# Performance work log

Hardware: AMD Instinct MI355X
Metric: run time of the kernel (lower is better)

## Reference

```python
import jax, jax.numpy as jnp
import numpy as np

NUM_NODES = 10000
NUM_EDGES = 640000
IN_CH = 128
HID = 128
OUT_CH = 1


def setup_inputs() -> dict:
    key = jax.random.key(0)
    ks = jax.random.split(key, 12)
    x = jax.random.normal(ks[0], (NUM_NODES, IN_CH), dtype=jnp.float32)
    edge_index = jax.random.randint(ks[1], (2, NUM_EDGES), 0, NUM_NODES, dtype=jnp.int64)
    edge_weight = jax.random.uniform(ks[2], (NUM_EDGES,), dtype=jnp.float32)
    s1 = 1.0 / np.sqrt(IN_CH)
    s2 = 1.0 / np.sqrt(HID)
    W1 = jax.random.uniform(ks[3], (HID, IN_CH), minval=-s1, maxval=s1, dtype=jnp.float32)
    b1 = jnp.zeros((HID,), dtype=jnp.float32)
    W2 = jax.random.uniform(ks[4], (HID, HID), minval=-s2, maxval=s2, dtype=jnp.float32)
    b2 = jnp.zeros((HID,), dtype=jnp.float32)
    sc = 1.0 / np.sqrt(HID * 3)
    conv_w = jax.random.uniform(ks[5], (HID, HID, 3), minval=-sc, maxval=sc, dtype=jnp.float32)
    conv_b = jax.random.uniform(ks[6], (HID,), minval=-sc, maxval=sc, dtype=jnp.float32)
    fc_w = jax.random.uniform(ks[7], (OUT_CH, HID), minval=-s2, maxval=s2, dtype=jnp.float32)
    fc_b = jax.random.uniform(ks[8], (OUT_CH,), minval=-s2, maxval=s2, dtype=jnp.float32)
    return {"x": x, "edge_index": edge_index, "edge_weight": edge_weight,
            "W1": W1, "b1": b1, "W2": W2, "b2": b2,
            "conv_w": conv_w, "conv_b": conv_b, "fc_w": fc_w, "fc_b": fc_b}


def _gcn_conv(x, row, col, norm, W, b):
    # PyG GCNConv: linear (no bias in lin), normalized scatter-add, then bias
    xw = x @ W.T                                   # [N, out]
    msg = xw[row] * norm[:, None]                  # gather + edge scale [E, out]
    out = jax.ops.segment_sum(msg, col, num_segments=NUM_NODES)
    return out + b


def reference(x, edge_index, edge_weight, W1, b1, W2, b2, conv_w, conv_b, fc_w, fc_b):
    # gcn_norm with self-loops (fill_value=1.0)
    loop = jnp.arange(NUM_NODES, dtype=edge_index.dtype)
    row = jnp.concatenate([edge_index[0], loop])
    col = jnp.concatenate([edge_index[1], loop])
    w = jnp.concatenate([edge_weight, jnp.ones((NUM_NODES,), dtype=edge_weight.dtype)])
    deg = jax.ops.segment_sum(w, col, num_segments=NUM_NODES)
    dinv = jnp.where(deg > 0, jax.lax.rsqrt(deg), 0.0)
    norm = dinv[row] * w * dinv[col]

    h = jax.nn.relu(_gcn_conv(x, row, col, norm, W1, b1))
    # dropout is identity in eval mode
    h = jax.nn.relu(_gcn_conv(h, row, col, norm, W2, b2))

    # temporal conv1d over node axis: [N,H] -> [1,H,N]
    hc = h.T[None, :, :]
    hc = jax.lax.conv_general_dilated(hc, conv_w, window_strides=(1,),
                                      padding='SAME',
                                      dimension_numbers=('NCH', 'OIH', 'NCH'))
    hc = hc + conv_b[None, :, None]
    h = hc[0].T                                    # [N, H]

    return (h @ fc_w.T + fc_b).squeeze()           # [N]
```

## Files before the change

kernel.cpp:

```cpp
#include <hip/hip_runtime.h>
#include <hip/hip_bf16.h>

#define N_NODES 10000
#define N_EDGES 640000
#define CH 128
#define NB 128
#define EPB (N_EDGES / NB)
#define NCHUNK 40

__global__ __launch_bounds__(256) void hist_kernel(const int* __restrict__ ei,
                                                   const float* __restrict__ ew,
                                                   int* __restrict__ hist,
                                                   float* __restrict__ dhist) {
    __shared__ int h[N_NODES];
    __shared__ float hf[N_NODES];
    int b = blockIdx.x, t = threadIdx.x;
    for (int i = t; i < N_NODES; i += 256) { h[i] = 0; hf[i] = 0.0f; }
    __syncthreads();
    int e0 = b * EPB;
    for (int i = t; i < EPB; i += 256) {
        int c = ei[N_EDGES + e0 + i];
        float w = ew[e0 + i];
        atomicAdd(&h[c], 1);
        atomicAdd(&hf[c], w);
    }
    __syncthreads();
    for (int i = t; i < N_NODES; i += 256) {
        hist[b * N_NODES + i] = h[i];
        dhist[b * N_NODES + i] = hf[i];
    }
}

__global__ __launch_bounds__(256) void reduce_kernel(const int* __restrict__ hist,
        const float* __restrict__ dhist, int* __restrict__ tot,
        float* __restrict__ dinv, int* __restrict__ csum,
        const float* __restrict__ conv_w, const float* __restrict__ conv_b,
        const float* __restrict__ fc_w, const float* __restrict__ fc_b,
        float* __restrict__ vbuf, float* __restrict__ c0) {
    int blk = blockIdx.x, t = threadIdx.x;
    if (blk == NCHUNK) {
        for (int i = t; i <= 384; i += 256) {
            if (i < 384) {
                float s = 0.0f;
                for (int o = 0; o < CH; ++o) s += fc_w[o] * conv_w[o * 384 + i];
                vbuf[i] = s;
            } else {
                float s = fc_b[0];
                for (int o = 0; o < CH; ++o) s += fc_w[o] * conv_b[o];
                *c0 = s;
            }
        }
        return;
    }
    int n = blk * 256 + t;
    int c = 0;
    if (n < N_NODES) {
        float d = 0.0f;
        #pragma unroll 4
        for (int b = 0; b < NB; ++b) {
            c += hist[b * N_NODES + n];
            d += dhist[b * N_NODES + n];
        }
        tot[n] = c;
        dinv[n] = rsqrtf(d + 1.0f);
    }
    __shared__ int wred[4];
    int lane = t & 63, wave = t >> 6;
    int s = c;
    #pragma unroll
    for (int off = 32; off > 0; off >>= 1) s += __shfl_down(s, off, 64);
    if (lane == 0) wred[wave] = s;
    __syncthreads();
    if (t == 0) csum[blk] = wred[0] + wred[1] + wred[2] + wred[3];
}

__global__ __launch_bounds__(256) void bofs_kernel(int* __restrict__ hist,
        const int* __restrict__ tot, const int* __restrict__ csum,
        int* __restrict__ offs) {
    __shared__ int lds_csum[NCHUNK];
    __shared__ int wsum[4];
    int blk = blockIdx.x, t = threadIdx.x;
    if (t < NCHUNK) lds_csum[t] = csum[t];
    __syncthreads();
    int base = 0;
    for (int i = 0; i < blk; ++i) base += lds_csum[i];
    int n = blk * 256 + t;
    int v = (n < N_NODES) ? tot[n] : 0;
    int lane = t & 63, wave = t >> 6;
    int s = v;
    #pragma unroll
    for (int off = 1; off < 64; off <<= 1) {
        int u = __shfl_up(s, off, 64);
        if (lane >= off) s += u;
    }
    if (lane == 63) wsum[wave] = s;
    __syncthreads();
    int wbase = 0;
    for (int i = 0; i < wave; ++i) wbase += wsum[i];
    if (n < N_NODES) {
        int run = base + wbase + s - v;
        offs[n] = run;
        for (int b = 0; b < NB; ++b) {
            int h = hist[b * N_NODES + n];
            hist[b * N_NODES + n] = run;
            run += h;
        }
    }
}

__global__ __launch_bounds__(256) void scatter_kernel(const int* __restrict__ ei,
        const float* __restrict__ ew, const float* __restrict__ dinv,
        const int* __restrict__ bofs, int2* __restrict__ erec) {
    __shared__ int cur[N_NODES];
    __shared__ float di[N_NODES];
    int b = blockIdx.x, t = threadIdx.x;
    for (int i = t; i < N_NODES; i += 256) {
        cur[i] = bofs[b * N_NODES + i];
        di[i] = dinv[i];
    }
    __syncthreads();
    int e0 = b * EPB;
    for (int i = t; i < EPB; i += 256) {
        int e = e0 + i;
        int r = ei[e];
        int c = ei[N_EDGES + e];
        int p = atomicAdd(&cur[c], 1);
        float v = di[r] * ew[e] * di[c];
        erec[p] = make_int2(r, __float_as_int(v));
    }
}

__global__ __launch_bounds__(256) void gemm128_kernel(const float* __restrict__ A,
                                                      const float* __restrict__ W,
                                                      float* __restrict__ out, int M) {
    __shared__ float As[32][68];
    __shared__ float Ws[32][132];
    int tid = threadIdx.x;
    int tx = tid & 31;
    int ty = tid >> 5;
    int row0 = blockIdx.x * 64;
    float acc[8][4] = {};
    for (int k0 = 0; k0 < 128; k0 += 32) {
        #pragma unroll
        for (int i = 0; i < 8; ++i) {
            int idx = tid + i * 256;
            int r = idx >> 5, k = idx & 31;
            int gr = row0 + r;
            As[k][r] = (gr < M) ? A[gr * CH + k0 + k] : 0.0f;
        }
        #pragma unroll
        for (int i = 0; i < 16; ++i) {
            int idx = tid + i * 256;
            int o = idx >> 5, k = idx & 31;
            Ws[k][o] = W[o * CH + k0 + k];
        }
        __syncthreads();
        #pragma unroll
        for (int kk = 0; kk < 32; ++kk) {
            float a[8], w[4];
            #pragma unroll
            for (int j = 0; j < 8; ++j) a[j] = As[kk][ty * 8 + j];
            #pragma unroll
            for (int c = 0; c < 4; ++c) w[c] = Ws[kk][tx * 4 + c];
            #pragma unroll
            for (int j = 0; j < 8; ++j)
                #pragma unroll
                for (int c = 0; c < 4; ++c)
                    acc[j][c] += a[j] * w[c];
        }
        __syncthreads();
    }
    #pragma unroll
    for (int j = 0; j < 8; ++j) {
        int gr = row0 + ty * 8 + j;
        if (gr < M) {
            float4 v = make_float4(acc[j][0], acc[j][1], acc[j][2], acc[j][3]);
            *reinterpret_cast<float4*>(&out[gr * CH + tx * 4]) = v;
        }
    }
}

__global__ __launch_bounds__(256) void agg_kernel(const float4* __restrict__ xw4,
        const int2* __restrict__ erec, const int* __restrict__ offs,
        const int* __restrict__ cnt, const float* __restrict__ dinv,
        const float4* __restrict__ bias4, float4* __restrict__ out4) {
    int l = threadIdx.x & 31;
    int g = threadIdx.x >> 5;
    int n = blockIdx.x * 8 + g;
    float d = dinv[n];
    float dd = d * d;
    float4 self = xw4[n * 32 + l];
    float4 acc = make_float4(dd * self.x, dd * self.y, dd * self.z, dd * self.w);
    int start = offs[n];
    int num = cnt[n];
    int i = 0;
    for (; i + 8 <= num; i += 8) {
        int2 r[8];
        #pragma unroll
        for (int j = 0; j < 8; ++j) r[j] = erec[start + i + j];
        float4 f[8];
        #pragma unroll
        for (int j = 0; j < 8; ++j) f[j] = xw4[r[j].x * 32 + l];
        #pragma unroll
        for (int j = 0; j < 8; ++j) {
            float v = __int_as_float(r[j].y);
            acc.x += v * f[j].x; acc.y += v * f[j].y;
            acc.z += v * f[j].z; acc.w += v * f[j].w;
        }
    }
    for (; i < num; ++i) {
        int2 r = erec[start + i];
        float4 f = xw4[r.x * 32 + l];
        float v = __int_as_float(r.y);
        acc.x += v * f.x; acc.y += v * f.y; acc.z += v * f.z; acc.w += v * f.w;
    }
    float4 bb = bias4[l];
    acc.x = fmaxf(acc.x + bb.x, 0.0f);
    acc.y = fmaxf(acc.y + bb.y, 0.0f);
    acc.z = fmaxf(acc.z + bb.z, 0.0f);
    acc.w = fmaxf(acc.w + bb.w, 0.0f);
    out4[n * 32 + l] = acc;
}

__global__ __launch_bounds__(128) void convfc_kernel(const float* __restrict__ h,
        const float* __restrict__ v, const float* __restrict__ c0,
        float* __restrict__ out, int N) {
    int n = blockIdx.x;
    int t = threadIdx.x;
    float p = 0.0f;
    if (n > 0)     p += h[(n - 1) * CH + t] * v[t * 3 + 0];
    p += h[n * CH + t] * v[t * 3 + 1];
    if (n < N - 1) p += h[(n + 1) * CH + t] * v[t * 3 + 2];
    #pragma unroll
    for (int off = 32; off > 0; off >>= 1) p += __shfl_down(p, off, 64);
    __shared__ float red[2];
    if ((t & 63) == 0) red[t >> 6] = p;
    __syncthreads();
    if (t == 0) out[n] = red[0] + red[1] + *c0;
}

extern "C" void kernel_launch(void* const* d_in, const int* in_sizes, int n_in,
                              void* d_out, int out_size, void* d_ws, size_t ws_size,
                              hipStream_t stream) {
    const float* x       = (const float*)d_in[0];
    const int*   ei      = (const int*)d_in[1];
    const float* ew      = (const float*)d_in[2];
    const float* W1      = (const float*)d_in[3];
    const float* b1      = (const float*)d_in[4];
    const float* W2      = (const float*)d_in[5];
    const float* b2      = (const float*)d_in[6];
    const float* conv_w  = (const float*)d_in[7];
    const float* conv_b  = (const float*)d_in[8];
    const float* fc_w    = (const float*)d_in[9];
    const float* fc_b    = (const float*)d_in[10];
    float* out = (float*)d_out;

    float* bufA   = (float*)d_ws;
    float* bufB   = bufA + N_NODES * CH;
    int2*  erec   = (int2*)(bufB + N_NODES * CH);
    int*   hist   = (int*)bufA;
    float* dhist  = (float*)erec;
    int*   tot    = (int*)(erec + N_EDGES);
    int*   offs   = tot + N_NODES;
    float* dinv   = (float*)(offs + N_NODES);
    float* vbuf   = dinv + N_NODES;
    float* c0     = vbuf + 384;
    int*   csum   = (int*)(c0 + 1);

    hist_kernel<<<NB, 256, 0, stream>>>(ei, ew, hist, dhist);
    reduce_kernel<<<NCHUNK + 1, 256, 0, stream>>>(hist, dhist, tot, dinv, csum,
                                                  conv_w, conv_b, fc_w, fc_b, vbuf, c0);
    bofs_kernel<<<NCHUNK, 256, 0, stream>>>(hist, tot, csum, offs);
    scatter_kernel<<<NB, 256, 0, stream>>>(ei, ew, dinv, hist, erec);

    const int gemm_grid = (N_NODES + 63) / 64;
    gemm128_kernel<<<gemm_grid, 256, 0, stream>>>(x, W1, bufA, N_NODES);
    agg_kernel<<<N_NODES / 8, 256, 0, stream>>>((const float4*)bufA, erec, offs, tot,
                                                dinv, (const float4*)b1, (float4*)bufB);
    gemm128_kernel<<<gemm_grid, 256, 0, stream>>>(bufB, W2, bufA, N_NODES);
    agg_kernel<<<N_NODES / 8, 256, 0, stream>>>((const float4*)bufA, erec, offs, tot,
                                                dinv, (const float4*)b2, (float4*)bufB);
    convfc_kernel<<<N_NODES, 128, 0, stream>>>(bufB, vbuf, c0, out, N_NODES);
}
```

Before: 227.4 us.

## Fuse all GCN stages into one persistent kernel with grid barriers

Replaces the nine separate kernel launches with a single persistent 256-block kernel that moves between phases using atomic-counter grid barriers. The first GEMM now runs alongside the degree histogram on the blocks that are otherwise idle, and the conv+fc tail is vectorised with float4 loads and 32-lane reductions. The aim is to remove launch gaps and idle tails between the small stages. In exchange, work per phase is limited to 256 blocks, seven spin barriers are added, and correctness depends on all 256 blocks being co-resident.

New measurement: 608.7 us. 2.68x slower.

```diff
diff --git a/kernel.cpp b/kernel.cpp
--- a/kernel.cpp
+++ b/kernel.cpp
@@ -1,144 +1,41 @@
 #include <hip/hip_runtime.h>
-#include <hip/hip_bf16.h>
 
 #define N_NODES 10000
 #define N_EDGES 640000
 #define CH 128
-#define NB 128
-#define EPB (N_EDGES / NB)
+#define NBLK 256
+#define NTHR 256
+#define NHB 128
+#define EPB (N_EDGES / NHB)
 #define NCHUNK 40
-
-__global__ __launch_bounds__(256) void hist_kernel(const int* __restrict__ ei,
-                                                   const float* __restrict__ ew,
-                                                   int* __restrict__ hist,
-                                                   float* __restrict__ dhist) {
-    __shared__ int h[N_NODES];
-    __shared__ float hf[N_NODES];
-    int b = blockIdx.x, t = threadIdx.x;
-    for (int i = t; i < N_NODES; i += 256) { h[i] = 0; hf[i] = 0.0f; }
+#define GTILES 157
+
+union SMem {
+    struct { int h[N_NODES]; float hf[N_NODES]; } hist;
+    struct { int cur[N_NODES]; float di[N_NODES]; } scat;
+    struct { float As[32][68]; float Ws[32][132]; } gemm;
+    struct { int csum[NCHUNK]; int wsum[4]; } scan;
+    int red[4];
+};
+
+__device__ __forceinline__ void gridbar(int* ctr, int target) {
+    __threadfence();
     __syncthreads();
-    int e0 = b * EPB;
-    for (int i = t; i < EPB; i += 256) {
-        int c = ei[N_EDGES + e0 + i];
-        float w = ew[e0 + i];
-        atomicAdd(&h[c], 1);
-        atomicAdd(&hf[c], w);
+    if (threadIdx.x == 0) {
+        atomicAdd(ctr, 1);
+        while (__hip_atomic_load(ctr, __ATOMIC_RELAXED, __HIP_MEMORY_SCOPE_AGENT) < target)
+            __builtin_amdgcn_s_sleep(2);
     }
     __syncthreads();
-    for (int i = t; i < N_NODES; i += 256) {
-        hist[b * N_NODES + i] = h[i];
-        dhist[b * N_NODES + i] = hf[i];
-    }
-}
-
-__global__ __launch_bounds__(256) void reduce_kernel(const int* __restrict__ hist,
-        const float* __restrict__ dhist, int* __restrict__ tot,
-        float* __restrict__ dinv, int* __restrict__ csum,
-        const float* __restrict__ conv_w, const float* __restrict__ conv_b,
-        const float* __restrict__ fc_w, const float* __restrict__ fc_b,
-        float* __restrict__ vbuf, float* __restrict__ c0) {
-    int blk = blockIdx.x, t = threadIdx.x;
-    if (blk == NCHUNK) {
-        for (int i = t; i <= 384; i += 256) {
-            if (i < 384) {
-                float s = 0.0f;
-                for (int o = 0; o < CH; ++o) s += fc_w[o] * conv_w[o * 384 + i];
-                vbuf[i] = s;
-            } else {
-                float s = fc_b[0];
-                for (int o = 0; o < CH; ++o) s += fc_w[o] * conv_b[o];
-                *c0 = s;
-            }
-        }
-        return;
-    }
-    int n = blk * 256 + t;
-    int c = 0;
-    if (n < N_NODES) {
-        float d = 0.0f;
-        #pragma unroll 4
-        for (int b = 0; b < NB; ++b) {
-            c += hist[b * N_NODES + n];
-            d += dhist[b * N_NODES + n];
-        }
-        tot[n] = c;
-        dinv[n] = rsqrtf(d + 1.0f);
-    }
-    __shared__ int wred[4];
-    int lane = t & 63, wave = t >> 6;
-    int s = c;
-    #pragma unroll
-    for (int off = 32; off > 0; off >>= 1) s += __shfl_down(s, off, 64);
-    if (lane == 0) wred[wave] = s;
-    __syncthreads();
-    if (t == 0) csum[blk] = wred[0] + wred[1] + wred[2] + wred[3];
-}
-
-__global__ __launch_bounds__(256) void bofs_kernel(int* __restrict__ hist,
-        const int* __restrict__ tot, const int* __restrict__ csum,
-        int* __restrict__ offs) {
-    __shared__ int lds_csum[NCHUNK];
-    __shared__ int wsum[4];
-    int blk = blockIdx.x, t = threadIdx.x;
-    if (t < NCHUNK) lds_csum[t] = csum[t];
-    __syncthreads();
-    int base = 0;
-    for (int i = 0; i < blk; ++i) base += lds_csum[i];
-    int n = blk * 256 + t;
-    int v = (n < N_NODES) ? tot[n] : 0;
-    int lane = t & 63, wave = t >> 6;
-    int s = v;
-    #pragma unroll
-    for (int off = 1; off < 64; off <<= 1) {
-        int u = __shfl_up(s, off, 64);
-        if (lane >= off) s += u;
-    }
-    if (lane == 63) wsum[wave] = s;
-    __syncthreads();
-    int wbase = 0;
-    for (int i = 0; i < wave; ++i) wbase += wsum[i];
-    if (n < N_NODES) {
-        int run = base + wbase + s - v;
-        offs[n] = run;
-        for (int b = 0; b < NB; ++b) {
-            int h = hist[b * N_NODES + n];
-            hist[b * N_NODES + n] = run;
-            run += h;
-        }
-    }
-}
-
-__global__ __launch_bounds__(256) void scatter_kernel(const int* __restrict__ ei,
-        const float* __restrict__ ew, const float* __restrict__ dinv,
-        const int* __restrict__ bofs, int2* __restrict__ erec) {
-    __shared__ int cur[N_NODES];
-    __shared__ float di[N_NODES];
-    int b = blockIdx.x, t = threadIdx.x;
-    for (int i = t; i < N_NODES; i += 256) {
-        cur[i] = bofs[b * N_NODES + i];
-        di[i] = dinv[i];
-    }
-    __syncthreads();
-    int e0 = b * EPB;
-    for (int i = t; i < EPB; i += 256) {
-        int e = e0 + i;
-        int r = ei[e];
-        int c = ei[N_EDGES + e];
-        int p = atomicAdd(&cur[c], 1);
-        float v = di[r] * ew[e] * di[c];
-        erec[p] = make_int2(r, __float_as_int(v));
-    }
-}
-
-__global__ __launch_bounds__(256) void gemm128_kernel(const float* __restrict__ A,
-                                                      const float* __restrict__ W,
-                                                      float* __restrict__ out, int M) {
-    __shared__ float As[32][68];
-    __shared__ float Ws[32][132];
+    __threadfence();
+}
+
+__device__ __forceinline__ void gemm_tile(const float* __restrict__ A,
+        const float* __restrict__ W, float* __restrict__ out, int tile, SMem& sm) {
     int tid = threadIdx.x;
     int tx = tid & 31;
     int ty = tid >> 5;
-    int row0 = blockIdx.x * 64;
+    int row0 = tile * 64;
     float acc[8][4] = {};
     for (int k0 = 0; k0 < 128; k0 += 32) {
         #pragma unroll
@@ -146,22 +43,22 @@
             int idx = tid + i * 256;
             int r = idx >> 5, k = idx & 31;
             int gr = row0 + r;
-            As[k][r] = (gr < M) ? A[gr * CH + k0 + k] : 0.0f;
+            sm.gemm.As[k][r] = (gr < N_NODES) ? A[gr * CH + k0 + k] : 0.0f;
         }
         #pragma unroll
         for (int i = 0; i < 16; ++i) {
             int idx = tid + i * 256;
             int o = idx >> 5, k = idx & 31;
-            Ws[k][o] = W[o * CH + k0 + k];
+            sm.gemm.Ws[k][o] = W[o * CH + k0 + k];
         }
         __syncthreads();
         #pragma unroll
         for (int kk = 0; kk < 32; ++kk) {
             float a[8], w[4];
             #pragma unroll
-            for (int j = 0; j < 8; ++j) a[j] = As[kk][ty * 8 + j];
-            #pragma unroll
-            for (int c = 0; c < 4; ++c) w[c] = Ws[kk][tx * 4 + c];
+            for (int j = 0; j < 8; ++j) a[j] = sm.gemm.As[kk][ty * 8 + j];
+            #pragma unroll
+            for (int c = 0; c < 4; ++c) w[c] = sm.gemm.Ws[kk][tx * 4 + c];
             #pragma unroll
             for (int j = 0; j < 8; ++j)
                 #pragma unroll
@@ -173,70 +70,215 @@
     #pragma unroll
     for (int j = 0; j < 8; ++j) {
         int gr = row0 + ty * 8 + j;
-        if (gr < M) {
+        if (gr < N_NODES) {
             float4 v = make_float4(acc[j][0], acc[j][1], acc[j][2], acc[j][3]);
             *reinterpret_cast<float4*>(&out[gr * CH + tx * 4]) = v;
         }
     }
 }
 
-__global__ __launch_bounds__(256) void agg_kernel(const float4* __restrict__ xw4,
+__device__ __forceinline__ void agg_phase(const float4* __restrict__ xw4,
         const int2* __restrict__ erec, const int* __restrict__ offs,
         const int* __restrict__ cnt, const float* __restrict__ dinv,
         const float4* __restrict__ bias4, float4* __restrict__ out4) {
     int l = threadIdx.x & 31;
     int g = threadIdx.x >> 5;
-    int n = blockIdx.x * 8 + g;
-    float d = dinv[n];
-    float dd = d * d;
-    float4 self = xw4[n * 32 + l];
-    float4 acc = make_float4(dd * self.x, dd * self.y, dd * self.z, dd * self.w);
-    int start = offs[n];
-    int num = cnt[n];
-    int i = 0;
-    for (; i + 8 <= num; i += 8) {
-        int2 r[8];
-        #pragma unroll
-        for (int j = 0; j < 8; ++j) r[j] = erec[start + i + j];
-        float4 f[8];
-        #pragma unroll
-        for (int j = 0; j < 8; ++j) f[j] = xw4[r[j].x * 32 + l];
-        #pragma unroll
-        for (int j = 0; j < 8; ++j) {
-            float v = __int_as_float(r[j].y);
-            acc.x += v * f[j].x; acc.y += v * f[j].y;
-            acc.z += v * f[j].z; acc.w += v * f[j].w;
-        }
-    }
-    for (; i < num; ++i) {
-        int2 r = erec[start + i];
-        float4 f = xw4[r.x * 32 + l];
-        float v = __int_as_float(r.y);
-        acc.x += v * f.x; acc.y += v * f.y; acc.z += v * f.z; acc.w += v * f.w;
-    }
-    float4 bb = bias4[l];
-    acc.x = fmaxf(acc.x + bb.x, 0.0f);
-    acc.y = fmaxf(acc.y + bb.y, 0.0f);
-    acc.z = fmaxf(acc.z + bb.z, 0.0f);
-    acc.w = fmaxf(acc.w + bb.w, 0.0f);
-    out4[n * 32 + l] = acc;
-}
-
-__global__ __launch_bounds__(128) void convfc_kernel(const float* __restrict__ h,
-        const float* __restrict__ v, const float* __restrict__ c0,
-        float* __restrict__ out, int N) {
-    int n = blockIdx.x;
-    int t = threadIdx.x;
-    float p = 0.0f;
-    if (n > 0)     p += h[(n - 1) * CH + t] * v[t * 3 + 0];
-    p += h[n * CH + t] * v[t * 3 + 1];
-    if (n < N - 1) p += h[(n + 1) * CH + t] * v[t * 3 + 2];
-    #pragma unroll
-    for (int off = 32; off > 0; off >>= 1) p += __shfl_down(p, off, 64);
-    __shared__ float red[2];
-    if ((t & 63) == 0) red[t >> 6] = p;
-    __syncthreads();
-    if (t == 0) out[n] = red[0] + red[1] + *c0;
+    for (int n = blockIdx.x * 8 + g; n < N_NODES; n += NBLK * 8) {
+        float d = dinv[n];
+        float dd = d * d;
+        float4 self = xw4[n * 32 + l];
+        float4 acc = make_float4(dd * self.x, dd * self.y, dd * self.z, dd * self.w);
+        int start = offs[n];
+        int num = cnt[n];
+        int i = 0;
+        for (; i + 8 <= num; i += 8) {
+            int2 r[8];
+            #pragma unroll
+            for (int j = 0; j < 8; ++j) r[j] = erec[start + i + j];
+            float4 f[8];
+            #pragma unroll
+            for (int j = 0; j < 8; ++j) f[j] = xw4[r[j].x * 32 + l];
+            #pragma unroll
+            for (int j = 0; j < 8; ++j) {
+                float v = __int_as_float(r[j].y);
+                acc.x += v * f[j].x; acc.y += v * f[j].y;
+                acc.z += v * f[j].z; acc.w += v * f[j].w;
+            }
+        }
+        for (; i < num; ++i) {
+            int2 r = erec[start + i];
+            float4 f = xw4[r.x * 32 + l];
+            float v = __int_as_float(r.y);
+            acc.x += v * f.x; acc.y += v * f.y; acc.z += v * f.z; acc.w += v * f.w;
+        }
+        float4 bb = bias4[l];
+        acc.x = fmaxf(acc.x + bb.x, 0.0f);
+        acc.y = fmaxf(acc.y + bb.y, 0.0f);
+        acc.z = fmaxf(acc.z + bb.z, 0.0f);
+        acc.w = fmaxf(acc.w + bb.w, 0.0f);
+        out4[n * 32 + l] = acc;
+    }
+}
+
+__global__ void init_ctr_kernel(int* ctr) { if (threadIdx.x == 0) *ctr = 0; }
+
+__global__ __launch_bounds__(NTHR) void mega_kernel(
+        const float* __restrict__ x, const int* __restrict__ ei,
+        const float* __restrict__ ew,
+        const float* __restrict__ W1, const float* __restrict__ b1,
+        const float* __restrict__ W2, const float* __restrict__ b2,
+        const float* __restrict__ conv_w, const float* __restrict__ conv_b,
+        const float* __restrict__ fc_w, const float* __restrict__ fc_b,
+        float* __restrict__ out,
+        float* __restrict__ xw1, float* __restrict__ h1,
+        float* __restrict__ xw2, float* __restrict__ h2,
+        int2* __restrict__ erec, int* __restrict__ hist, float* __restrict__ dhist,
+        int* __restrict__ tot, int* __restrict__ offs, float* __restrict__ dinv,
+        int* __restrict__ csum, float* __restrict__ vbuf, float* __restrict__ c0,
+        int* __restrict__ barctr) {
+    __shared__ SMem sm;
+    const int b = blockIdx.x, t = threadIdx.x;
+
+    if (b < NHB) {
+        for (int i = t; i < N_NODES; i += NTHR) { sm.hist.h[i] = 0; sm.hist.hf[i] = 0.0f; }
+        __syncthreads();
+        int e0 = b * EPB;
+        for (int i = t; i < EPB; i += NTHR) {
+            int c = ei[N_EDGES + e0 + i];
+            float w = ew[e0 + i];
+            atomicAdd(&sm.hist.h[c], 1);
+            atomicAdd(&sm.hist.hf[c], w);
+        }
+        __syncthreads();
+        for (int i = t; i < N_NODES; i += NTHR) {
+            hist[b * N_NODES + i] = sm.hist.h[i];
+            dhist[b * N_NODES + i] = sm.hist.hf[i];
+        }
+    } else {
+        int bb = b - NHB;
+        gemm_tile(x, W1, xw1, bb, sm);
+        if (bb + NHB < GTILES) gemm_tile(x, W1, xw1, bb + NHB, sm);
+        if (b == NBLK - 1) {
+            for (int i = t; i <= 384; i += NTHR) {
+                if (i < 384) {
+                    float s = 0.0f;
+                    for (int o = 0; o < CH; ++o) s += fc_w[o] * conv_w[o * 384 + i];
+                    vbuf[i] = s;
+                } else {
+                    float s = fc_b[0];
+                    for (int o = 0; o < CH; ++o) s += fc_w[o] * conv_b[o];
+                    *c0 = s;
+                }
+            }
+        }
+    }
+    gridbar(barctr, NBLK * 1);
+
+    if (b < NCHUNK) {
+        int n = b * NTHR + t;
+        int c = 0;
+        if (n < N_NODES) {
+            float d = 0.0f;
+            #pragma unroll 4
+            for (int bb = 0; bb < NHB; ++bb) {
+                c += hist[bb * N_NODES + n];
+                d += dhist[bb * N_NODES + n];
+            }
+            tot[n] = c;
+            dinv[n] = rsqrtf(d + 1.0f);
+        }
+        int lane = t & 63, wave = t >> 6;
+        int s = c;
+        #pragma unroll
+        for (int off = 32; off > 0; off >>= 1) s += __shfl_down(s, off, 64);
+        if (lane == 0) sm.red[wave] = s;
+        __syncthreads();
+        if (t == 0) csum[b] = sm.red[0] + sm.red[1] + sm.red[2] + sm.red[3];
+    }
+    gridbar(barctr, NBLK * 2);
+
+    if (b < NCHUNK) {
+        if (t < NCHUNK) sm.scan.csum[t] = csum[t];
+        __syncthreads();
+        int base = 0;
+        for (int i = 0; i < b; ++i) base += sm.scan.csum[i];
+        int n = b * NTHR + t;
+        int v = (n < N_NODES) ? tot[n] : 0;
+        int lane = t & 63, wave = t >> 6;
+        int s = v;
+        #pragma unroll
+        for (int off = 1; off < 64; off <<= 1) {
+            int u = __shfl_up(s, off, 64);
+            if (lane >= off) s += u;
+        }
+        if (lane == 63) sm.scan.wsum[wave] = s;
+        __syncthreads();
+        int wbase = 0;
+        for (int i = 0; i < wave; ++i) wbase += sm.scan.wsum[i];
+        if (n < N_NODES) {
+            int run = base + wbase + s - v;
+            offs[n] = run;
+            for (int bb = 0; bb < NHB; ++bb) {
+                int hh = hist[bb * N_NODES + n];
+                hist[bb * N_NODES + n] = run;
+                run += hh;
+            }
+        }
+    }
+    gridbar(barctr, NBLK * 3);
+
+    if (b < NHB) {
+        for (int i = t; i < N_NODES; i += NTHR) {
+            sm.scat.cur[i] = hist[b * N_NODES + i];
+            sm.scat.di[i] = dinv[i];
+        }
+        __syncthreads();
+        int e0 = b * EPB;
+        for (int i = t; i < EPB; i += NTHR) {
+            int e = e0 + i;
+            int r = ei[e];
+            int c = ei[N_EDGES + e];
+            int p = atomicAdd(&sm.scat.cur[c], 1);
+            float v = sm.scat.di[r] * ew[e] * sm.scat.di[c];
+            erec[p] = make_int2(r, __float_as_int(v));
+        }
+    }
+    gridbar(barctr, NBLK * 4);
+
+    agg_phase((const float4*)xw1, erec, offs, tot, dinv, (const float4*)b1, (float4*)h1);
+    gridbar(barctr, NBLK * 5);
+
+    if (b < GTILES) gemm_tile(h1, W2, xw2, b, sm);
+    gridbar(barctr, NBLK * 6);
+
+    agg_phase((const float4*)xw2, erec, offs, tot, dinv, (const float4*)b2, (float4*)h2);
+    gridbar(barctr, NBLK * 7);
+
+    {
+        int l = t & 31;
+        int g = t >> 5;
+        const float4* h4 = (const float4*)h2;
+        float v00 = vbuf[(4 * l + 0) * 3 + 0], v01 = vbuf[(4 * l + 0) * 3 + 1], v02 = vbuf[(4 * l + 0) * 3 + 2];
+        float v10 = vbuf[(4 * l + 1) * 3 + 0], v11 = vbuf[(4 * l + 1) * 3 + 1], v12 = vbuf[(4 * l + 1) * 3 + 2];
+        float v20 = vbuf[(4 * l + 2) * 3 + 0], v21 = vbuf[(4 * l + 2) * 3 + 1], v22 = vbuf[(4 * l + 2) * 3 + 2];
+        float v30 = vbuf[(4 * l + 3) * 3 + 0], v31 = vbuf[(4 * l + 3) * 3 + 1], v32 = vbuf[(4 * l + 3) * 3 + 2];
+        float cc = *c0;
+        for (int n = b * 8 + g; n < N_NODES; n += NBLK * 8) {
+            float4 hm = h4[n * 32 + l];
+            float p = hm.x * v01 + hm.y * v11 + hm.z * v21 + hm.w * v31;
+            if (n > 0) {
+                float4 ha = h4[(n - 1) * 32 + l];
+                p += ha.x * v00 + ha.y * v10 + ha.z * v20 + ha.w * v30;
+            }
+            if (n < N_NODES - 1) {
+                float4 hb = h4[(n + 1) * 32 + l];
+                p += hb.x * v02 + hb.y * v12 + hb.z * v22 + hb.w * v32;
+            }
+            #pragma unroll
+            for (int off = 16; off > 0; off >>= 1) p += __shfl_down(p, off, 32);
+            if (l == 0) out[n] = p + cc;
+        }
+    }
 }
 
 extern "C" void kernel_launch(void* const* d_in, const int* in_sizes, int n_in,
@@ -255,30 +297,24 @@
     const float* fc_b    = (const float*)d_in[10];
     float* out = (float*)d_out;
 
-    float* bufA   = (float*)d_ws;
-    float* bufB   = bufA + N_NODES * CH;
-    int2*  erec   = (int2*)(bufB + N_NODES * CH);
-    int*   hist   = (int*)bufA;
-    float* dhist  = (float*)erec;
-    int*   tot    = (int*)(erec + N_EDGES);
-    int*   offs   = tot + N_NODES;
-    float* dinv   = (float*)(offs + N_NODES);
-    float* vbuf   = dinv + N_NODES;
-    float* c0     = vbuf + 384;
-    int*   csum   = (int*)(c0 + 1);
-
-    hist_kernel<<<NB, 256, 0, stream>>>(ei, ew, hist, dhist);
-    reduce_kernel<<<NCHUNK + 1, 256, 0, stream>>>(hist, dhist, tot, dinv, csum,
-                                                  conv_w, conv_b, fc_w, fc_b, vbuf, c0);
-    bofs_kernel<<<NCHUNK, 256, 0, stream>>>(hist, tot, csum, offs);
-    scatter_kernel<<<NB, 256, 0, stream>>>(ei, ew, dinv, hist, erec);
-
-    const int gemm_grid = (N_NODES + 63) / 64;
-    gemm128_kernel<<<gemm_grid, 256, 0, stream>>>(x, W1, bufA, N_NODES);
-    agg_kernel<<<N_NODES / 8, 256, 0, stream>>>((const float4*)bufA, erec, offs, tot,
-                                                dinv, (const float4*)b1, (float4*)bufB);
-    gemm128_kernel<<<gemm_grid, 256, 0, stream>>>(bufB, W2, bufA, N_NODES);
-    agg_kernel<<<N_NODES / 8, 256, 0, stream>>>((const float4*)bufA, erec, offs, tot,
-                                                dinv, (const float4*)b2, (float4*)bufB);
-    convfc_kernel<<<N_NODES, 128, 0, stream>>>(bufB, vbuf, c0, out, N_NODES);
-}
+    float* xw1   = (float*)d_ws;
+    float* h1    = xw1 + N_NODES * CH;
+    float* xw2   = h1 + N_NODES * CH;
+    float* h2    = xw2 + N_NODES * CH;
+    int2*  erec  = (int2*)(h2 + N_NODES * CH);
+    int*   hist  = (int*)(erec + N_EDGES);
+    float* dhist = (float*)(hist + NHB * N_NODES);
+    int*   tot   = (int*)(dhist + NHB * N_NODES);
+    int*   offs  = tot + N_NODES;
+    float* dinv  = (float*)(offs + N_NODES);
+    int*   csum  = (int*)(dinv + N_NODES);
+    float* vbuf  = (float*)(csum + NCHUNK);
+    float* c0    = vbuf + 384;
+    int*   barctr = (int*)(c0 + 1);
+
+    init_ctr_kernel<<<1, 64, 0, stream>>>(barctr);
+    mega_kernel<<<NBLK, NTHR, 0, stream>>>(x, ei, ew, W1, b1, W2, b2,
+                                           conv_w, conv_b, fc_w, fc_b, out,
+                                           xw1, h1, xw2, h2, erec, hist, dhist,
+                                           tot, offs, dinv, csum, vbuf, c0, barctr);
+}
```
